# Kernel tuning notes

Hardware: AMD Instinct MI355X
Metric: run time of the kernel (lower is better)

Reference implementation:

```python
import jax, jax.numpy as jnp
import numpy as np

DIM = 768
HEADS = 12
HEAD_DIM = DIM // HEADS
RANK = 8
SCALING = 1.0 / RANK  # lora_alpha / r
SCALE = HEAD_DIM ** -0.5


def setup_inputs() -> dict:
    key = jax.random.key(0)
    ks = jax.random.split(key, 14)
    B, N, D, r = 4, 1024, DIM, RANK
    s = lambda k, shape, sd=0.02: jax.random.normal(k, shape, jnp.float32) * sd
    return {
        "x": jax.random.normal(ks[0], (B, N, D), jnp.float32),
        "qkv_w": s(ks[1], (3 * D, D)),
        "qkv_b": s(ks[2], (3 * D,)),
        "q_base_w": s(ks[3], (D, D)),
        "q_base_b": s(ks[4], (D,)),
        "q_A": s(ks[5], (r, D), 1.0 / r),
        "q_B": s(ks[6], (D, r)),
        "k_base_w": s(ks[7], (D, D)),
        "k_base_b": s(ks[8], (D,)),
        "k_A": s(ks[9], (r, D), 1.0 / r),
        "k_B": s(ks[10], (D, r)),
        "proj_w": s(ks[11], (D, D)),
        "proj_b": s(ks[12], (D,)),
    }


def _lora_linear(x, w, b, A, Bm):
    # base linear + LoRA delta: x@w.T + b + (x@A.T)@B.T * scaling
    return x @ w.T + b + ((x @ A.T) @ Bm.T) * SCALING


def reference(x, qkv_w, qkv_b, q_base_w, q_base_b, q_A, q_B,
              k_base_w, k_base_b, k_A, k_B, proj_w, proj_b):
    B, N, D = x.shape
    H, hd = HEADS, HEAD_DIM
    qkv = (x @ qkv_w.T + qkv_b).reshape(B, N, 3, H, hd).transpose(2, 0, 3, 1, 4)
    q, k, v = qkv[0], qkv[1], qkv[2]  # [B,H,N,hd]
    q_delta = _lora_linear(x, q_base_w, q_base_b, q_A, q_B).reshape(B, N, H, hd).transpose(0, 2, 1, 3)
    k_delta = _lora_linear(x, k_base_w, k_base_b, k_A, k_B).reshape(B, N, H, hd).transpose(0, 2, 1, 3)
    q = q + q_delta
    k = k + k_delta
    attn = jnp.einsum('bhnd,bhmd->bhnm', q, k) * SCALE
    attn = jax.nn.softmax(attn, axis=-1)
    out = jnp.einsum('bhnm,bhmd->bhnd', attn, v)
    out = out.transpose(0, 2, 1, 3).reshape(B, N, D)
    return out @ proj_w.T + proj_b
```

## Files before the change

kernel.cpp:

```cpp
#include <hip/hip_runtime.h>
#include <hip/hip_bf16.h>


typedef _Float16 half8 __attribute__((ext_vector_type(8)));
typedef float f32x4 __attribute__((ext_vector_type(4)));

typedef __attribute__((address_space(3))) unsigned int lds_u32;
typedef __attribute__((address_space(1))) const unsigned int glob_u32;

__device__ __forceinline__ void glds16(const void* g, void* l) {
    __builtin_amdgcn_global_load_lds((glob_u32*)g, (lds_u32*)l, 16, 0, 0);
}

__device__ __forceinline__ float pk2f16(float a, float b) {
    return __builtin_bit_cast(float, __builtin_amdgcn_cvt_pkrtz(a, b));
}

#define SMSCALE 0.18033688011112042f

constexpr size_t OFF_WX = 0;
constexpr size_t OFF_PH = OFF_WX + (size_t)2304*800*2;
constexpr size_t OFF_XE = OFF_PH + (size_t)768*768*2;
constexpr size_t OFF_QH = OFF_XE + (size_t)4096*800*2;
constexpr size_t OFF_KH = OFF_QH + (size_t)48*1024*64*2;
constexpr size_t OFF_VH = OFF_KH + (size_t)48*1024*64*2;
constexpr size_t OFF_VT = OFF_VH + (size_t)48*1024*64*2;
constexpr size_t OFF_AO = OFF_VT + (size_t)48*1024*64*2;

__global__ __launch_bounds__(256)
void prep(const float* __restrict__ qkv_w, const float* __restrict__ qkv_b,
          const float* __restrict__ qw, const float* __restrict__ qbias,
          const float* __restrict__ kw, const float* __restrict__ kbias,
          const float* __restrict__ proj_w, const float* __restrict__ qB,
          const float* __restrict__ kB,
          _Float16* __restrict__ Wx, _Float16* __restrict__ Ph) {
    const int t = threadIdx.x, bb = blockIdx.x;
    if (bb < 2304) {
        const int n = bb;
        const float rs = (n < 768) ? SMSCALE : 1.0f;
        const float* wsrc = qkv_w + (size_t)n * 768;
        const float* fold = (n < 768) ? (qw + (size_t)n * 768)
                          : (n < 1536 ? (kw + (size_t)(n - 768) * 768) : nullptr);
        _Float16* dst = Wx + (size_t)n * 800;
#pragma unroll
        for (int i = 0; i < 3; ++i) {
            const int c = t + i * 256;
            float v = wsrc[c];
            if (fold) v += fold[c];
            dst[c] = (_Float16)(v * rs);
        }
        if (t < 32) {
            float v = 0.f;
            if (t < 8)       { if (n < 768) v = rs * 0.125f * qB[n * 8 + t]; }
            else if (t < 16) { if (n >= 768 && n < 1536) v = 0.125f * kB[(size_t)(n - 768) * 8 + (t - 8)]; }
            else if (t == 16) v = rs * (qkv_b[n] + (n < 768 ? qbias[n] : (n < 1536 ? kbias[n - 768] : 0.f)));
            dst[768 + t] = (_Float16)v;
        }
    } else {
        const size_t idx = ((size_t)(bb - 2304) * 256 + t) * 4;
        const float4 v = *(const float4*)(proj_w + idx);
        _Float16* d = Ph + idx;
        d[0] = (_Float16)v.x; d[1] = (_Float16)v.y;
        d[2] = (_Float16)v.z; d[3] = (_Float16)v.w;
    }
}

__global__ __launch_bounds__(256)
void lora_xa(const float* __restrict__ x, const float* __restrict__ qA,
             const float* __restrict__ kA, _Float16* __restrict__ Xe) {
    __shared__ float As_[16][772];
    __shared__ float xs[8][768];
    const int t = threadIdx.x, m0 = blockIdx.x * 8;

#pragma unroll
    for (int i = t * 4; i < 12288; i += 1024) {
        const int r = i / 768, c = i - r * 768;
        const float4 v = *(const float4*)((r < 8 ? qA + (size_t)r * 768 : kA + (size_t)(r - 8) * 768) + c);
        As_[r][c] = v.x; As_[r][c + 1] = v.y; As_[r][c + 2] = v.z; As_[r][c + 3] = v.w;
    }
#pragma unroll
    for (int i = t * 4; i < 6144; i += 1024) {
        const int r = i / 768, c = i - r * 768;
        const float4 v = *(const float4*)(x + (size_t)(m0 + r) * 768 + c);
        xs[r][c] = v.x; xs[r][c + 1] = v.y; xs[r][c + 2] = v.z; xs[r][c + 3] = v.w;
        _Float16* d = Xe + (size_t)(m0 + r) * 800 + c;
        d[0] = (_Float16)v.x; d[1] = (_Float16)v.y; d[2] = (_Float16)v.z; d[3] = (_Float16)v.w;
    }
    __syncthreads();

    const int j = t >> 4, lane = t & 15;
#pragma unroll
    for (int r = 0; r < 8; ++r) {
        float acc = 0.f;
        for (int k = lane; k < 768; k += 16) acc += xs[r][k] * As_[j][k];
        acc += __shfl_xor(acc, 1); acc += __shfl_xor(acc, 2);
        acc += __shfl_xor(acc, 4); acc += __shfl_xor(acc, 8);
        if (lane == 0) Xe[(size_t)(m0 + r) * 800 + 768 + j] = (_Float16)acc;
    }
    if (t < 128) {
        const int r = t >> 4, c = t & 15;
        Xe[(size_t)(m0 + r) * 800 + 784 + c] = (c == 0) ? (_Float16)1.f : (_Float16)0.f;
    }
}

template<int BM, int BN, int MODE>
__global__ __launch_bounds__(256)
void gemm_h(const _Float16* __restrict__ A, const _Float16* __restrict__ Bw,
            const int lda, const int ldb, const int nsteps,
            const float* __restrict__ bias,
            _Float16* __restrict__ Oq, _Float16* __restrict__ Ok, _Float16* __restrict__ Ov,
            float* __restrict__ Co) {
    constexpr int CA = BM / 16, CB = BN / 16;
    constexpr int MI = BM / 32, NI = BN / 32;
    __shared__ __align__(16) _Float16 As[2][BM * 32];
    __shared__ __align__(16) _Float16 Bs[2][BN * 32];
    const int t = threadIdx.x;
    const int w = t >> 6, l = t & 63;
    const int l15 = l & 15, lg = l >> 4;
    const int wm = w >> 1, wn = w & 1;

    const int gx = gridDim.x;
    int lin = blockIdx.y * gx + blockIdx.x;
    lin = (lin & 7) * ((gx * gridDim.y) >> 3) + (lin >> 3);
    const int n0 = (lin % gx) * BN, m0 = (lin / gx) * BM;

    const _Float16* gA[CA / 4];
    const _Float16* gB[CB / 4];
#pragma unroll
    for (int i = 0; i < CA / 4; ++i)
        gA[i] = A + (size_t)(m0 + (w * (CA / 4) + i) * 16 + l15) * lda + lg * 8;
#pragma unroll
    for (int i = 0; i < CB / 4; ++i)
        gB[i] = Bw + (size_t)(n0 + (w * (CB / 4) + i) * 16 + l15) * ldb + lg * 8;

    f32x4 acc[MI][NI];
#pragma unroll
    for (int mi = 0; mi < MI; ++mi)
#pragma unroll
        for (int ni = 0; ni < NI; ++ni) acc[mi][ni] = 0.f;

#pragma unroll
    for (int i = 0; i < CA / 4; ++i) { glds16(gA[i], &As[0][(w * (CA / 4) + i) * 512]); gA[i] += 32; }
#pragma unroll
    for (int i = 0; i < CB / 4; ++i) { glds16(gB[i], &Bs[0][(w * (CB / 4) + i) * 512]); gB[i] += 32; }
    __syncthreads();

    for (int s = 0; s < nsteps; ++s) {
        const int cur = s & 1;
        if (s + 1 < nsteps) {
#pragma unroll
            for (int i = 0; i < CA / 4; ++i) { glds16(gA[i], &As[cur ^ 1][(w * (CA / 4) + i) * 512]); gA[i] += 32; }
#pragma unroll
            for (int i = 0; i < CB / 4; ++i) { glds16(gB[i], &Bs[cur ^ 1][(w * (CB / 4) + i) * 512]); gB[i] += 32; }
        }
        half8 a[MI], b[NI];
#pragma unroll
        for (int mi = 0; mi < MI; ++mi) a[mi] = *(const half8*)&As[cur][(wm * MI + mi) * 512 + l * 8];
#pragma unroll
        for (int ni = 0; ni < NI; ++ni) b[ni] = *(const half8*)&Bs[cur][(wn * NI + ni) * 512 + l * 8];
#pragma unroll
        for (int mi = 0; mi < MI; ++mi)
#pragma unroll
            for (int ni = 0; ni < NI; ++ni)
                acc[mi][ni] = __builtin_amdgcn_mfma_f32_16x16x32_f16(a[mi], b[ni], acc[mi][ni], 0, 0, 0);
        __syncthreads();
    }

    if (MODE == 0) {
#pragma unroll
        for (int mi = 0; mi < MI; ++mi)
#pragma unroll
            for (int reg = 0; reg < 4; ++reg) {
                const int m = m0 + wm * (BM / 2) + mi * 16 + lg * 4 + reg;
                const int b_ = m >> 10, nn = m & 1023;
#pragma unroll
                for (int ni = 0; ni < NI; ++ni) {
                    const int n = n0 + wn * (BN / 2) + ni * 16 + l15;
                    const int sel = (n >= 1536) ? 2 : (n >= 768 ? 1 : 0);
                    const int jj = n - sel * 768;
                    const int h = jj >> 6, d = jj & 63;
                    _Float16* dst = (sel == 0) ? Oq : (sel == 1 ? Ok : Ov);
                    dst[(((size_t)(b_ * 12 + h)) * 1024 + nn) * 64 + d] = (_Float16)acc[mi][ni][reg];
                }
            }
    } else {
#pragma unroll
        for (int mi = 0; mi < MI; ++mi)
#pragma unroll
            for (int reg = 0; reg < 4; ++reg) {
                const int m = m0 + wm * (BM / 2) + mi * 16 + lg * 4 + reg;
#pragma unroll
                for (int ni = 0; ni < NI; ++ni) {
                    const int n = n0 + wn * (BN / 2) + ni * 16 + l15;
                    Co[(size_t)m * 768 + n] = acc[mi][ni][reg] + bias[n];
                }
            }
    }
}

__global__ __launch_bounds__(256)
void vt_k(const _Float16* __restrict__ Vh, _Float16* __restrict__ Vt) {
    __shared__ __align__(16) _Float16 tile[64][72];
    const int t = threadIdx.x;
    const int nb = blockIdx.x, bh = blockIdx.y;
    {
        const int key = t >> 2, h0 = (t & 3) * 16;
        const size_t src = ((size_t)(bh * 1024 + nb * 64 + key)) * 64 + h0;
        *(half8*)&tile[key][h0]     = *(const half8*)&Vh[src];
        *(half8*)&tile[key][h0 + 8] = *(const half8*)&Vh[src + 8];
    }
    __syncthreads();
    const int hd = t >> 2, k0 = (t & 3) * 16;
    half8 a, b;
#pragma unroll
    for (int j = 0; j < 8; ++j) { a[j] = tile[k0 + j][hd]; b[j] = tile[k0 + 8 + j][hd]; }
    const size_t dst = ((size_t)(bh * 64 + hd)) * 1024 + nb * 64 + k0;
    *(half8*)&Vt[dst]     = a;
    *(half8*)&Vt[dst + 8] = b;
}

#define STAGEK(kbt, buf) { \
_Pragma("unroll") \
    for (int i = 0; i < 4; ++i) { \
        const int c = w * 4 + i; \
        glds16(Kp + (size_t)((kbt) * 64 + (c >> 1) * 16 + l15) * 64 + (c & 1) * 32 + lg * 8, &Ks[buf][c * 512]); \
    } }
#define STAGEV(kbt, buf) { \
_Pragma("unroll") \
    for (int i = 0; i < 4; ++i) { \
        const int c = w * 4 + i; \
        glds16(Vp + (size_t)((c >> 1) * 16 + l15) * 1024 + (kbt) * 64 + (c & 1) * 32 + lg * 8, &Vs[buf][c * 512]); \
    } }
#define QK(buf, s) { \
    half8 kreg[8]; \
_Pragma("unroll") \
    for (int c = 0; c < 8; ++c) kreg[c] = *(const half8*)&Ks[buf][c * 512 + l * 8]; \
_Pragma("unroll") \
    for (int mi = 0; mi < 2; ++mi) \
_Pragma("unroll") \
        for (int nj = 0; nj < 4; ++nj) { \
            s[mi][nj] = 0.f; \
_Pragma("unroll") \
            for (int kh = 0; kh < 2; ++kh) \
                s[mi][nj] = __builtin_amdgcn_mfma_f32_16x16x32_f16(kreg[nj * 2 + kh], qf[mi][kh], s[mi][nj], 0, 0, 0); \
        } }
#define EXPP(ph, s) { \
_Pragma("unroll") \
    for (int mi = 0; mi < 2; ++mi) { \
        float ls = 0.f; \
_Pragma("unroll") \
        for (int nj = 0; nj < 4; ++nj) { \
            const float p0 = __builtin_amdgcn_exp2f(s[mi][nj][0]); \
            const float p1 = __builtin_amdgcn_exp2f(s[mi][nj][1]); \
            const float p2 = __builtin_amdgcn_exp2f(s[mi][nj][2]); \
            const float p3 = __builtin_amdgcn_exp2f(s[mi][nj][3]); \
            ls += (p0 + p1) + (p2 + p3); \
            float2 pk; \
            pk.x = pk2f16(p0, p1); \
            pk.y = pk2f16(p2, p3); \
            const int off = (mi * 2 + (nj >> 1)) * 512 + (2 * (nj & 1) + (lg >> 1)) * 128 \
                          + l15 * 8 + 4 * (lg & 1); \
            *(float2*)&Ps[w][ph][off] = pk; \
        } \
        lsum[mi] += ls; \
    } }
#define PV(ph, buf) { \
    half8 pf[2][2]; \
_Pragma("unroll") \
    for (int mi = 0; mi < 2; ++mi) \
_Pragma("unroll") \
        for (int kh = 0; kh < 2; ++kh) \
            pf[mi][kh] = *(const half8*)&Ps[w][ph][(mi * 2 + kh) * 512 + l * 8]; \
_Pragma("unroll") \
    for (int fj = 0; fj < 4; ++fj) \
_Pragma("unroll") \
        for (int kh = 0; kh < 2; ++kh) { \
            const half8 vf = *(const half8*)&Vs[buf][(fj * 2 + kh) * 512 + l * 8]; \
_Pragma("unroll") \
            for (int mi = 0; mi < 2; ++mi) \
                o[mi][fj] = __builtin_amdgcn_mfma_f32_16x16x32_f16(pf[mi][kh], vf, o[mi][fj], 0, 0, 0); \
        } }

__global__ __launch_bounds__(128)
void attn5(const _Float16* __restrict__ Q, const _Float16* __restrict__ K,
           const _Float16* __restrict__ Vt, _Float16* __restrict__ AO) {
    __shared__ __align__(16) _Float16 Ks[2][4096];
    __shared__ __align__(16) _Float16 Vs[2][4096];
    __shared__ __align__(16) _Float16 Ps[2][2][2048];
    __shared__ float sums[2][32];
    const int t = threadIdx.x;
    const int w = t >> 6, l = t & 63;
    const int l15 = l & 15, lg = l >> 4;

    int lin = blockIdx.y * 16 + blockIdx.x;
    lin = (lin & 7) * 96 + (lin >> 3);
    const int qb = lin & 15, bh = lin >> 4;

    const _Float16* Qp = Q  + (size_t)bh * 65536;
    const _Float16* Kp = K  + (size_t)bh * 65536;
    const _Float16* Vp = Vt + (size_t)bh * 65536;

    STAGEK(0, 0); STAGEK(1, 1); STAGEV(0, 0);
    half8 qf[2][2];
#pragma unroll
    for (int mi = 0; mi < 2; ++mi)
#pragma unroll
        for (int kh = 0; kh < 2; ++kh)
            qf[mi][kh] = *(const half8*)&Qp[(size_t)(qb * 64 + w * 32 + mi * 16 + l15) * 64 + kh * 32 + lg * 8];

    f32x4 o[2][4];
#pragma unroll
    for (int mi = 0; mi < 2; ++mi)
#pragma unroll
        for (int fj = 0; fj < 4; ++fj) o[mi][fj] = 0.f;
    float lsum[2] = {0.f, 0.f};
    __syncthreads();

    {
        f32x4 s[2][4];
        QK(0, s);
        EXPP(0, s);
    }
    __syncthreads();

    for (int kb = 0; kb < 15; ++kb) {
        const int cb = kb & 1, nb = cb ^ 1;
        if (kb + 2 < 16) STAGEK(kb + 2, cb);
        STAGEV(kb + 1, nb);
        f32x4 s[2][4];
        __builtin_amdgcn_s_setprio(1);
        QK(nb, s);
        PV(cb, cb);
        __builtin_amdgcn_s_setprio(0);
        EXPP(nb, s);
        __syncthreads();
    }
    PV(1, 1);

#pragma unroll
    for (int mi = 0; mi < 2; ++mi) {
        float tot = lsum[mi];
        tot += __shfl_xor(tot, 16);
        tot += __shfl_xor(tot, 32);
        if (lg == 0) sums[w][mi * 16 + l15] = tot;
    }
    __builtin_amdgcn_wave_barrier();

    const int b_ = bh / 12, h = bh % 12;
#pragma unroll
    for (int mi = 0; mi < 2; ++mi)
#pragma unroll
        for (int reg = 0; reg < 4; ++reg) {
            const float inv = 1.f / sums[w][mi * 16 + lg * 4 + reg];
            const int tok = qb * 64 + w * 32 + mi * 16 + lg * 4 + reg;
            const size_t base = ((size_t)(b_ * 1024 + tok)) * 768 + h * 64;
#pragma unroll
            for (int fj = 0; fj < 4; ++fj)
                AO[base + fj * 16 + l15] = (_Float16)(o[mi][fj][reg] * inv);
        }
}

extern "C" void kernel_launch(void* const* d_in, const int* in_sizes, int n_in,
                              void* d_out, int out_size, void* d_ws, size_t ws_size,
                              hipStream_t stream) {
    (void)in_sizes; (void)n_in; (void)out_size; (void)ws_size;
    const float* x      = (const float*)d_in[0];
    const float* qkv_w  = (const float*)d_in[1];
    const float* qkv_b  = (const float*)d_in[2];
    const float* q_bw   = (const float*)d_in[3];
    const float* q_bb   = (const float*)d_in[4];
    const float* q_A    = (const float*)d_in[5];
    const float* q_B    = (const float*)d_in[6];
    const float* k_bw   = (const float*)d_in[7];
    const float* k_bb   = (const float*)d_in[8];
    const float* k_A    = (const float*)d_in[9];
    const float* k_B    = (const float*)d_in[10];
    const float* proj_w = (const float*)d_in[11];
    const float* proj_b = (const float*)d_in[12];
    float* out = (float*)d_out;
    char*  ws  = (char*)d_ws;

    _Float16* Wx = (_Float16*)(ws + OFF_WX);
    _Float16* Ph = (_Float16*)(ws + OFF_PH);
    _Float16* Xe = (_Float16*)(ws + OFF_XE);
    _Float16* Qh = (_Float16*)(ws + OFF_QH);
    _Float16* Kh = (_Float16*)(ws + OFF_KH);
    _Float16* Vh = (_Float16*)(ws + OFF_VH);
    _Float16* Vt = (_Float16*)(ws + OFF_VT);
    _Float16* AO = (_Float16*)(ws + OFF_AO);

    prep<<<dim3(2880), dim3(256), 0, stream>>>(qkv_w, qkv_b, q_bw, q_bb, k_bw, k_bb,
                                               proj_w, q_B, k_B, Wx, Ph);
    lora_xa<<<dim3(512), dim3(256), 0, stream>>>(x, q_A, k_A, Xe);
    gemm_h<128, 128, 0><<<dim3(18, 32), dim3(256), 0, stream>>>(
        Xe, Wx, 800, 800, 25, nullptr, Qh, Kh, Vh, nullptr);
    vt_k<<<dim3(16, 48), dim3(256), 0, stream>>>(Vh, Vt);
    attn5<<<dim3(16, 48), dim3(128), 0, stream>>>(Qh, Kh, Vt, AO);
    gemm_h<64, 128, 1><<<dim3(6, 64), dim3(256), 0, stream>>>(
        AO, Ph, 768, 768, 24, proj_b, nullptr, nullptr, nullptr, out);
}
```

Before: 116.7 us.

## Fuse V transpose into QKV GEMM epilogue and retile GEMMs to BN=96

```diff
diff --git a/kernel.cpp b/kernel.cpp
--- a/kernel.cpp
+++ b/kernel.cpp
@@ -23,8 +23,7 @@
 constexpr size_t OFF_XE = OFF_PH + (size_t)768*768*2;
 constexpr size_t OFF_QH = OFF_XE + (size_t)4096*800*2;
 constexpr size_t OFF_KH = OFF_QH + (size_t)48*1024*64*2;
-constexpr size_t OFF_VH = OFF_KH + (size_t)48*1024*64*2;
-constexpr size_t OFF_VT = OFF_VH + (size_t)48*1024*64*2;
+constexpr size_t OFF_VT = OFF_KH + (size_t)48*1024*64*2;
 constexpr size_t OFF_AO = OFF_VT + (size_t)48*1024*64*2;
 
 __global__ __launch_bounds__(256)
@@ -110,7 +109,7 @@
             const float* __restrict__ bias,
             _Float16* __restrict__ Oq, _Float16* __restrict__ Ok, _Float16* __restrict__ Ov,
             float* __restrict__ Co) {
-    constexpr int CA = BM / 16, CB = BN / 16;
+    constexpr int CA = BM / 16, CB = BN / 16, CT = CA + CB;
     constexpr int MI = BM / 32, NI = BN / 32;
     __shared__ __align__(16) _Float16 As[2][BM * 32];
     __shared__ __align__(16) _Float16 Bs[2][BN * 32];
@@ -124,14 +123,8 @@
     lin = (lin & 7) * ((gx * gridDim.y) >> 3) + (lin >> 3);
     const int n0 = (lin % gx) * BN, m0 = (lin / gx) * BM;
 
-    const _Float16* gA[CA / 4];
-    const _Float16* gB[CB / 4];
-#pragma unroll
-    for (int i = 0; i < CA / 4; ++i)
-        gA[i] = A + (size_t)(m0 + (w * (CA / 4) + i) * 16 + l15) * lda + lg * 8;
-#pragma unroll
-    for (int i = 0; i < CB / 4; ++i)
-        gB[i] = Bw + (size_t)(n0 + (w * (CB / 4) + i) * 16 + l15) * ldb + lg * 8;
+    const _Float16* Abase = A + (size_t)(m0 + l15) * lda + lg * 8;
+    const _Float16* Bbase = Bw + (size_t)(n0 + l15) * ldb + lg * 8;
 
     f32x4 acc[MI][NI];
 #pragma unroll
@@ -140,18 +133,21 @@
         for (int ni = 0; ni < NI; ++ni) acc[mi][ni] = 0.f;
 
 #pragma unroll
-    for (int i = 0; i < CA / 4; ++i) { glds16(gA[i], &As[0][(w * (CA / 4) + i) * 512]); gA[i] += 32; }
-#pragma unroll
-    for (int i = 0; i < CB / 4; ++i) { glds16(gB[i], &Bs[0][(w * (CB / 4) + i) * 512]); gB[i] += 32; }
+    for (int c = w; c < CT; c += 4) {
+        if (c < CA) glds16(Abase + (size_t)(c * 16) * lda, &As[0][c * 512]);
+        else        glds16(Bbase + (size_t)((c - CA) * 16) * ldb, &Bs[0][(c - CA) * 512]);
+    }
     __syncthreads();
 
     for (int s = 0; s < nsteps; ++s) {
         const int cur = s & 1;
         if (s + 1 < nsteps) {
-#pragma unroll
-            for (int i = 0; i < CA / 4; ++i) { glds16(gA[i], &As[cur ^ 1][(w * (CA / 4) + i) * 512]); gA[i] += 32; }
-#pragma unroll
-            for (int i = 0; i < CB / 4; ++i) { glds16(gB[i], &Bs[cur ^ 1][(w * (CB / 4) + i) * 512]); gB[i] += 32; }
+            const int ko = (s + 1) * 32;
+#pragma unroll
+            for (int c = w; c < CT; c += 4) {
+                if (c < CA) glds16(Abase + (size_t)(c * 16) * lda + ko, &As[cur ^ 1][c * 512]);
+                else        glds16(Bbase + (size_t)((c - CA) * 16) * ldb + ko, &Bs[cur ^ 1][(c - CA) * 512]);
+            }
         }
         half8 a[MI], b[NI];
 #pragma unroll
@@ -167,22 +163,38 @@
     }
 
     if (MODE == 0) {
-#pragma unroll
-        for (int mi = 0; mi < MI; ++mi)
-#pragma unroll
-            for (int reg = 0; reg < 4; ++reg) {
-                const int m = m0 + wm * (BM / 2) + mi * 16 + lg * 4 + reg;
-                const int b_ = m >> 10, nn = m & 1023;
+        const int sel = (n0 >= 1536) ? 2 : (n0 >= 768 ? 1 : 0);
+        const int b_ = m0 >> 10, nnb = m0 & 1023;
+        if (sel < 2) {
+            _Float16* dst = (sel == 0) ? Oq : Ok;
+            const int jb = n0 - sel * 768;
+#pragma unroll
+            for (int mi = 0; mi < MI; ++mi)
+#pragma unroll
+                for (int reg = 0; reg < 4; ++reg) {
+                    const int nn = nnb + wm * (BM / 2) + mi * 16 + lg * 4 + reg;
+#pragma unroll
+                    for (int ni = 0; ni < NI; ++ni) {
+                        const int jj = jb + wn * (BN / 2) + ni * 16 + l15;
+                        const int h = jj >> 6, d = jj & 63;
+                        dst[(((size_t)(b_ * 12 + h)) * 1024 + nn) * 64 + d] = (_Float16)acc[mi][ni][reg];
+                    }
+                }
+        } else {
+#pragma unroll
+            for (int mi = 0; mi < MI; ++mi) {
+                const int nn = nnb + wm * (BM / 2) + mi * 16 + lg * 4;
 #pragma unroll
                 for (int ni = 0; ni < NI; ++ni) {
-                    const int n = n0 + wn * (BN / 2) + ni * 16 + l15;
-                    const int sel = (n >= 1536) ? 2 : (n >= 768 ? 1 : 0);
-                    const int jj = n - sel * 768;
+                    const int jj = (n0 - 1536) + wn * (BN / 2) + ni * 16 + l15;
                     const int h = jj >> 6, d = jj & 63;
-                    _Float16* dst = (sel == 0) ? Oq : (sel == 1 ? Ok : Ov);
-                    dst[(((size_t)(b_ * 12 + h)) * 1024 + nn) * 64 + d] = (_Float16)acc[mi][ni][reg];
+                    float2 pv;
+                    pv.x = pk2f16(acc[mi][ni][0], acc[mi][ni][1]);
+                    pv.y = pk2f16(acc[mi][ni][2], acc[mi][ni][3]);
+                    *(float2*)&Ov[(((size_t)(b_ * 12 + h)) * 64 + d) * 1024 + nn] = pv;
                 }
             }
+        }
     } else {
 #pragma unroll
         for (int mi = 0; mi < MI; ++mi)
@@ -196,27 +208,6 @@
                 }
             }
     }
-}
-
-__global__ __launch_bounds__(256)
-void vt_k(const _Float16* __restrict__ Vh, _Float16* __restrict__ Vt) {
-    __shared__ __align__(16) _Float16 tile[64][72];
-    const int t = threadIdx.x;
-    const int nb = blockIdx.x, bh = blockIdx.y;
-    {
-        const int key = t >> 2, h0 = (t & 3) * 16;
-        const size_t src = ((size_t)(bh * 1024 + nb * 64 + key)) * 64 + h0;
-        *(half8*)&tile[key][h0]     = *(const half8*)&Vh[src];
-        *(half8*)&tile[key][h0 + 8] = *(const half8*)&Vh[src + 8];
-    }
-    __syncthreads();
-    const int hd = t >> 2, k0 = (t & 3) * 16;
-    half8 a, b;
-#pragma unroll
-    for (int j = 0; j < 8; ++j) { a[j] = tile[k0 + j][hd]; b[j] = tile[k0 + 8 + j][hd]; }
-    const size_t dst = ((size_t)(bh * 64 + hd)) * 1024 + nb * 64 + k0;
-    *(half8*)&Vt[dst]     = a;
-    *(half8*)&Vt[dst + 8] = b;
 }
 
 #define STAGEK(kbt, buf) { \
@@ -385,17 +376,15 @@
     _Float16* Xe = (_Float16*)(ws + OFF_XE);
     _Float16* Qh = (_Float16*)(ws + OFF_QH);
     _Float16* Kh = (_Float16*)(ws + OFF_KH);
-    _Float16* Vh = (_Float16*)(ws + OFF_VH);
     _Float16* Vt = (_Float16*)(ws + OFF_VT);
     _Float16* AO = (_Float16*)(ws + OFF_AO);
 
     prep<<<dim3(2880), dim3(256), 0, stream>>>(qkv_w, qkv_b, q_bw, q_bb, k_bw, k_bb,
                                                proj_w, q_B, k_B, Wx, Ph);
     lora_xa<<<dim3(512), dim3(256), 0, stream>>>(x, q_A, k_A, Xe);
-    gemm_h<128, 128, 0><<<dim3(18, 32), dim3(256), 0, stream>>>(
-        Xe, Wx, 800, 800, 25, nullptr, Qh, Kh, Vh, nullptr);
-    vt_k<<<dim3(16, 48), dim3(256), 0, stream>>>(Vh, Vt);
+    gemm_h<128, 96, 0><<<dim3(24, 32), dim3(256), 0, stream>>>(
+        Xe, Wx, 800, 800, 25, nullptr, Qh, Kh, Vt, nullptr);
     attn5<<<dim3(16, 48), dim3(128), 0, stream>>>(Qh, Kh, Vt, AO);
-    gemm_h<64, 128, 1><<<dim3(6, 64), dim3(256), 0, stream>>>(
+    gemm_h<64, 96, 1><<<dim3(8, 64), dim3(256), 0, stream>>>(
         AO, Ph, 768, 768, 24, proj_b, nullptr, nullptr, nullptr, out);
 }
```

Measured after the change: 110.9 us. 5.0% less time.
